# Kernel tuning notes

Hardware: AMD Instinct MI355X
Metric: run time of the kernel (lower is better)

## Reference

```python
import jax, jax.numpy as jnp
import numpy as np

T, B, H = 1024, 32, 1024

def setup_inputs() -> dict:
    key = jax.random.key(0)
    k1, k2, k3 = jax.random.split(key, 3)
    f = jax.random.uniform(k1, (T, B, H), dtype=jnp.float32)  # forget gates in [0,1]
    x = jax.random.normal(k2, (T, B, H), dtype=jnp.float32)
    hidden_init = jax.random.normal(k3, (B, H), dtype=jnp.float32)
    return {"f": f, "x": x, "hidden_init": hidden_init}

def reference(f, x, hidden_init):
    # h_t = f_t * x_t + (1 - f_t) * h_{t-1}, left-to-right (direction=0)
    fx = f * x  # [T, B, H]
    def step(h_prev, inputs):
        f_t, fx_t = inputs
        h_t = fx_t + (1.0 - f_t) * h_prev
        return h_t, h_t
    _, hs = jax.lax.scan(step, hidden_init, (f, fx))
    return hs  # [T, B, H]
```

## Files before the change

### kernel.cpp

```cpp
#include <hip/hip_runtime.h>


constexpr int UNROLL = 16;

__global__ __launch_bounds__(64) void forgetmult_kernel(
    const float* __restrict__ f, const float* __restrict__ x,
    const float* __restrict__ h0, float* __restrict__ out,
    int T, int BH)
{
    const int c = blockIdx.x * 64 + threadIdx.x;
    if (c >= BH) return;

    float h = h0[c];
    const float* fp = f + c;
    const float* xp = x + c;
    float*       op = out + c;
    const size_t stride = (size_t)BH;

    for (int t0 = 0; t0 < T; t0 += UNROLL) {
        float fv[UNROLL], xv[UNROLL];
        #pragma unroll
        for (int u = 0; u < UNROLL; ++u) {
            const size_t off = (size_t)(t0 + u) * stride;
            fv[u] = fp[off];
            xv[u] = xp[off];
        }
        #pragma unroll
        for (int u = 0; u < UNROLL; ++u) {
            h = fmaf(fv[u], xv[u] - h, h);
            op[(size_t)(t0 + u) * stride] = h;
        }
    }
}

extern "C" void kernel_launch(void* const* d_in, const int* in_sizes, int n_in,
                              void* d_out, int out_size, void* d_ws, size_t ws_size,
                              hipStream_t stream) {
    const float* f  = (const float*)d_in[0];
    const float* x  = (const float*)d_in[1];
    const float* h0 = (const float*)d_in[2];
    float* out = (float*)d_out;

    const int BH = in_sizes[2];
    const int T  = in_sizes[0] / BH;

    const int block = 64;
    const int grid  = (BH + block - 1) / block;
    forgetmult_kernel<<<grid, block, 0, stream>>>(f, x, h0, out, T, BH);
}
```

Measured before the change: 307.3 us.

## Double-buffer time-step loads and use nontemporal loads and stores

The recurrence loop now uses two register buffers, so the next block of 16 time steps is loaded while the current block is computed, keeping more loads in flight per thread. Loads and stores also use nontemporal builtins to avoid polluting the cache with streaming data. A scalar tail loop handles leftover steps. The cost is higher register use per thread, and the nontemporal hints may or may not help bandwidth.

Result: faster. 294.0 us (-4.3%).

```diff
diff --git a/kernel.cpp b/kernel.cpp
--- a/kernel.cpp
+++ b/kernel.cpp
@@ -1,9 +1,9 @@
 #include <hip/hip_runtime.h>
 
 
-constexpr int UNROLL = 16;
+constexpr int U = 16;
 
-__global__ __launch_bounds__(64) void forgetmult_kernel(
+__global__ __launch_bounds__(64, 1) void forgetmult_kernel(
     const float* __restrict__ f, const float* __restrict__ x,
     const float* __restrict__ h0, float* __restrict__ out,
     int T, int BH)
@@ -11,25 +11,59 @@
     const int c = blockIdx.x * 64 + threadIdx.x;
     if (c >= BH) return;
 
-    float h = h0[c];
+    const size_t stride = (size_t)BH;
     const float* fp = f + c;
     const float* xp = x + c;
     float*       op = out + c;
-    const size_t stride = (size_t)BH;
 
-    for (int t0 = 0; t0 < T; t0 += UNROLL) {
-        float fv[UNROLL], xv[UNROLL];
+    float h = h0[c];
+
+    float fA[U], xA[U], fB[U], xB[U];
+
+    const int nblk = T / (2 * U);
+    int t = 0;
+
+    if (nblk > 0) {
         #pragma unroll
-        for (int u = 0; u < UNROLL; ++u) {
-            const size_t off = (size_t)(t0 + u) * stride;
-            fv[u] = fp[off];
-            xv[u] = xp[off];
+        for (int u = 0; u < U; ++u) {
+            const size_t off = (size_t)u * stride;
+            fA[u] = __builtin_nontemporal_load(fp + off);
+            xA[u] = __builtin_nontemporal_load(xp + off);
         }
-        #pragma unroll
-        for (int u = 0; u < UNROLL; ++u) {
-            h = fmaf(fv[u], xv[u] - h, h);
-            op[(size_t)(t0 + u) * stride] = h;
+        for (int b = 0; b < nblk; ++b) {
+            #pragma unroll
+            for (int u = 0; u < U; ++u) {
+                const size_t off = (size_t)(t + U + u) * stride;
+                fB[u] = __builtin_nontemporal_load(fp + off);
+                xB[u] = __builtin_nontemporal_load(xp + off);
+            }
+            #pragma unroll
+            for (int u = 0; u < U; ++u) {
+                h = fmaf(fA[u], xA[u] - h, h);
+                __builtin_nontemporal_store(h, op + (size_t)(t + u) * stride);
+            }
+            if (b + 1 < nblk) {
+                #pragma unroll
+                for (int u = 0; u < U; ++u) {
+                    const size_t off = (size_t)(t + 2 * U + u) * stride;
+                    fA[u] = __builtin_nontemporal_load(fp + off);
+                    xA[u] = __builtin_nontemporal_load(xp + off);
+                }
+            }
+            #pragma unroll
+            for (int u = 0; u < U; ++u) {
+                h = fmaf(fB[u], xB[u] - h, h);
+                __builtin_nontemporal_store(h, op + (size_t)(t + U + u) * stride);
+            }
+            t += 2 * U;
         }
+    }
+
+    for (; t < T; ++t) {
+        const float fv = fp[(size_t)t * stride];
+        const float xv = xp[(size_t)t * stride];
+        h = fmaf(fv, xv - h, h);
+        op[(size_t)t * stride] = h;
     }
 }
 
```
